# Performance work log

Hardware: AMD Instinct MI355X
Metric: run time of the kernel (lower is better)

The kernel has to match this reference:

```python
import jax, jax.numpy as jnp
import numpy as np

K_CLUSTERS = 64   # hardcoded k=64 in get_kmenas_prototypes
KM_ITERS = 10     # KMeans(max_iter=10)


def _kmeans_one_hot(x):
    """x: (B, N, C) points. Returns one-hot cluster masks (B, K, N)."""
    B, N, C = x.shape
    init_idx = jnp.round(jnp.linspace(0, N - 1, K_CLUSTERS)).astype(jnp.int32)

    def per_item(pts):  # (N, C)
        p2 = (pts * pts).sum(-1)  # (N,)

        def assign(cent):
            c2 = (cent * cent).sum(-1)
            d = p2[:, None] + c2[None, :] - 2.0 * (pts @ cent.T)  # (N, K)
            return jnp.argmin(d, axis=1)

        def step(i, cent):
            lab = assign(cent)
            oh = jax.nn.one_hot(lab, K_CLUSTERS, dtype=pts.dtype)  # (N, K)
            cnt = oh.sum(0)
            sums = oh.T @ pts  # (K, C)
            return jnp.where(cnt[:, None] > 0, sums / jnp.maximum(cnt, 1.0)[:, None], cent)

        cent = jax.lax.fori_loop(0, KM_ITERS, step, pts[init_idx])
        lab = assign(cent)
        return jax.nn.one_hot(lab, K_CLUSTERS, dtype=pts.dtype).T  # (K, N)

    return jax.vmap(per_item)(x)


def reference(target, ref, sqz_w, sqz_b, slot_w, slot_b, Wq, Wk, Wv, Wo):
    B, Cin, H, W = target.shape
    Cout = sqz_w.shape[0]
    R = ref.shape[0]
    HW = H * W

    # 1x1 convs
    sqz_target = jnp.einsum('bchw,oc->bohw', target, sqz_w) + sqz_b[None, :, None, None]
    slot_target = jnp.einsum('bchw,oc->bohw', target, slot_w) + slot_b[None, :, None, None]

    xt = sqz_target.reshape(B, Cout, HW)  # (B, C, HW)

    # KMeans prototypes (clustering mask is detached in the original)
    mask = jax.lax.stop_gradient(_kmeans_one_hot(xt.transpose(0, 2, 1)))  # (B, K, HW)
    target_pt = jnp.einsum('bkn,bcn->bkc', mask, xt)  # (B, K, C)

    # slot prototypes: softmax over slot/channel dim (dim=1)
    ss = jax.nn.softmax(slot_target.reshape(B, -1, HW), axis=1)  # (B, S, HW)
    slot_pt = jnp.einsum('bsn,bcn->bsc', ss, xt)  # (B, S, C)
    slot_mask = ss.reshape(B, -1, H, W)

    # ref prototypes: mask = feature itself, softmax over spatial dim (dim=2)
    sqz_ref = jnp.einsum('rbchw,oc->rbohw', ref, sqz_w) + sqz_b[None, None, :, None, None]
    xr = sqz_ref.reshape(R, B, Cout, HW)
    ssr = jax.nn.softmax(xr, axis=3)
    ref_pt = jnp.einsum('rbcn,rbdn->rbcd', ssr, xr)  # (R, B, C, C)

    # Feature_Aggregation_Transformer: cross-attention, queries = kmeans tokens,
    # kv = flattened ref prototype tokens (b, R*C, C)
    kv = ref_pt.transpose(1, 0, 2, 3).reshape(B, R * Cout, Cout)
    q = target_pt @ Wq
    k = kv @ Wk
    v = kv @ Wv
    scale = 1.0 / jnp.sqrt(jnp.asarray(Cout, q.dtype))
    attn = jax.nn.softmax(jnp.einsum('bqc,bkc->bqk', q, k) * scale, axis=-1)
    agg_pt = jnp.einsum('bqk,bkc->bqc', attn, v) @ Wo + target_pt  # (B, K, C)

    return (sqz_target, agg_pt, ref_pt, slot_pt, slot_mask)


def setup_inputs() -> dict:
    key = jax.random.key(0)
    ks = jax.random.split(key, 12)
    B, Cin, Cout, S, H, W, R = 8, 512, 128, 16, 64, 64, 3
    w = lambda k, shp: (jax.random.normal(k, shp, dtype=jnp.float32) * 0.02)
    return {
        'target': jax.random.normal(ks[0], (B, Cin, H, W), dtype=jnp.float32),
        'ref': jax.random.normal(ks[1], (R, B, Cin, H, W), dtype=jnp.float32),
        'sqz_w': w(ks[2], (Cout, Cin)),
        'sqz_b': jnp.zeros((Cout,), dtype=jnp.float32),
        'slot_w': w(ks[3], (S, Cin)),
        'slot_b': jnp.zeros((S,), dtype=jnp.float32),
        'Wq': w(ks[4], (Cout, Cout)),
        'Wk': w(ks[5], (Cout, Cout)),
        'Wv': w(ks[6], (Cout, Cout)),
        'Wo': w(ks[7], (Cout, Cout)),
    }
```

## Files before the change

### kernel.cpp

```cpp
#include <hip/hip_runtime.h>

#define NB 8
#define CIN 512
#define CO 128
#define NS 16
#define NHW 4096
#define NR 3
#define NK 64
#define KMITERS 10

typedef __attribute__((ext_vector_type(8))) short s16x8;
typedef __attribute__((ext_vector_type(4))) float f32x4;

static __device__ __forceinline__ void bsplit(float x, short& h, short& l) {
    union { float f; unsigned u; } a; a.f = x;
    h = (short)(a.u >> 16);
    union { unsigned u; float f; } hf; hf.u = a.u & 0xFFFF0000u;
    union { float f; unsigned u; } r; r.f = x - hf.f;
    l = (short)(r.u >> 16);
}

__global__ __launch_bounds__(256) void conv_mfma(const float* __restrict__ X,
    const float* __restrict__ Wt, const float* __restrict__ bias, float* __restrict__ out)
{
    __shared__ short sWh[128 * 40];
    __shared__ short sWl[128 * 40];
    __shared__ float sX[32 * 133];
    const int g = blockIdx.y;
    const int n0 = blockIdx.x * 128;
    const int tid = threadIdx.x;
    const int lane = tid & 63, w = tid >> 6;
    const int l15 = lane & 15, quad = lane >> 4;
    const int wm = (w & 1) * 64, wn = (w >> 1) * 64;

    f32x4 acc[4][4];
#pragma unroll
    for (int i = 0; i < 4; ++i)
#pragma unroll
        for (int j = 0; j < 4; ++j) acc[i][j] = (f32x4){0.f, 0.f, 0.f, 0.f};

    for (int c0 = 0; c0 < CIN; c0 += 32) {
        if (c0) __syncthreads();
#pragma unroll
        for (int r = 0; r < 4; ++r) {
            int e = r * 1024 + tid * 4;
            int m = e >> 5, cc = e & 31;
            const float4 wv = *(const float4*)&Wt[(size_t)m * CIN + c0 + cc];
            short h0, l0, h1, l1, h2, l2, h3, l3;
            bsplit(wv.x, h0, l0); bsplit(wv.y, h1, l1);
            bsplit(wv.z, h2, l2); bsplit(wv.w, h3, l3);
            *(short4*)&sWh[m * 40 + cc] = make_short4(h0, h1, h2, h3);
            *(short4*)&sWl[m * 40 + cc] = make_short4(l0, l1, l2, l3);
        }
#pragma unroll
        for (int r = 0; r < 4; ++r) {
            int e = r * 1024 + tid * 4;
            int k = e >> 7, n = e & 127;
            const float4 xv = *(const float4*)&X[((size_t)g * CIN + c0 + k) * NHW + n0 + n];
            float* p = &sX[k * 133 + n];
            p[0] = xv.x; p[1] = xv.y; p[2] = xv.z; p[3] = xv.w;
        }
        __syncthreads();

        s16x8 ah[4], al[4];
#pragma unroll
        for (int mt = 0; mt < 4; ++mt) {
            int m = wm + mt * 16 + l15;
            ah[mt] = *(const s16x8*)&sWh[m * 40 + quad * 8];
            al[mt] = *(const s16x8*)&sWl[m * 40 + quad * 8];
        }
#pragma unroll
        for (int nt = 0; nt < 4; ++nt) {
            int n = wn + nt * 16 + l15;
            s16x8 bh, bl;
#pragma unroll
            for (int jj = 0; jj < 8; ++jj) {
                float xv = sX[(quad * 8 + jj) * 133 + n];
                short h, l; bsplit(xv, h, l);
                bh[jj] = h; bl[jj] = l;
            }
#pragma unroll
            for (int mt = 0; mt < 4; ++mt) {
                acc[mt][nt] = __builtin_amdgcn_mfma_f32_16x16x32_bf16(ah[mt], bh, acc[mt][nt], 0, 0, 0);
                acc[mt][nt] = __builtin_amdgcn_mfma_f32_16x16x32_bf16(ah[mt], bl, acc[mt][nt], 0, 0, 0);
                acc[mt][nt] = __builtin_amdgcn_mfma_f32_16x16x32_bf16(al[mt], bh, acc[mt][nt], 0, 0, 0);
            }
        }
    }
#pragma unroll
    for (int mt = 0; mt < 4; ++mt) {
#pragma unroll
        for (int reg = 0; reg < 4; ++reg) {
            int m = wm + mt * 16 + quad * 4 + reg;
            float bv = bias[m];
#pragma unroll
            for (int nt = 0; nt < 4; ++nt) {
                int n = wn + nt * 16 + l15;
                out[((size_t)g * CO + m) * NHW + n0 + n] = acc[mt][nt][reg] + bv;
            }
        }
    }
}

template<int BM, int BN, int BK, int TM, int TN>
__global__ __launch_bounds__(256) void conv1x1(const float* __restrict__ X,
    const float* __restrict__ Wt, const float* __restrict__ bias,
    float* __restrict__ outf)
{
    static_assert(TM == 4 && (TN == 4 || TN == 8), "mapping assumes TM=4");
    __shared__ float sW[BK][BM + 4];
    __shared__ float sX2[BK][BN + 4];
    const int g  = blockIdx.z;
    const int m0 = blockIdx.y * BM;
    const int n0 = blockIdx.x * BN;
    const int tid = threadIdx.x;
    constexpr int NTH_N = BN / TN;
    const int tn = tid % NTH_N;
    const int tm = tid / NTH_N;
    const int O = gridDim.y * BM;
    const int cb0 = tn * 4;
    const int cb1 = BN / 2 + tn * 4;

    float acc[TM][TN];
#pragma unroll
    for (int i = 0; i < TM; ++i)
#pragma unroll
        for (int j = 0; j < TN; ++j) acc[i][j] = 0.f;

    for (int c0 = 0; c0 < CIN; c0 += BK) {
        if (c0) __syncthreads();
        constexpr int F4R = BK / 4;
        for (int idx4 = tid; idx4 < BM * F4R; idx4 += 256) {
            int m = idx4 / F4R, cw = (idx4 % F4R) * 4;
            const float4 wv = *(const float4*)&Wt[(size_t)(m0 + m) * CIN + c0 + cw];
            sW[cw][m] = wv.x; sW[cw + 1][m] = wv.y;
            sW[cw + 2][m] = wv.z; sW[cw + 3][m] = wv.w;
        }
        constexpr int F4N = BN / 4;
        for (int idx4 = tid; idx4 < BK * F4N; idx4 += 256) {
            int k = idx4 / F4N, n4 = (idx4 % F4N) * 4;
            *(float4*)&sX2[k][n4] =
                *(const float4*)&X[((size_t)g * CIN + c0 + k) * NHW + n0 + n4];
        }
        __syncthreads();
#pragma unroll
        for (int k = 0; k < BK; ++k) {
            float a[TM], bb[TN];
            *(float4*)&a[0] = *(const float4*)&sW[k][tm * 4];
            *(float4*)&bb[0] = *(const float4*)&sX2[k][cb0];
            if constexpr (TN == 8)
                *(float4*)&bb[4] = *(const float4*)&sX2[k][cb1];
#pragma unroll
            for (int i = 0; i < TM; ++i)
#pragma unroll
                for (int j = 0; j < TN; ++j) acc[i][j] = fmaf(a[i], bb[j], acc[i][j]);
        }
    }
#pragma unroll
    for (int i = 0; i < TM; ++i) {
        int m = m0 + tm * 4 + i;
        float bv = bias[m];
        float4 o0;
        o0.x = acc[i][0] + bv; o0.y = acc[i][1] + bv;
        o0.z = acc[i][2] + bv; o0.w = acc[i][3] + bv;
        *(float4*)&outf[((size_t)g * O + m) * NHW + n0 + cb0] = o0;
        if constexpr (TN == 8) {
            float4 o1;
            o1.x = acc[i][4] + bv; o1.y = acc[i][5] + bv;
            o1.z = acc[i][6] + bv; o1.w = acc[i][7] + bv;
            *(float4*)&outf[((size_t)g * O + m) * NHW + n0 + cb1] = o1;
        }
    }
}

__global__ void km_init(const float* __restrict__ xt, float* __restrict__ cent) {
    int idx = blockIdx.x * 256 + threadIdx.x;
    if (idx >= NB * NK * CO) return;
    int c = idx % CO;
    int k = (idx / CO) % NK;
    int b = idx / (CO * NK);
    cent[idx] = xt[((size_t)b * CO + c) * NHW + 65 * k];
}

__global__ __launch_bounds__(1024) void km_label(const float* __restrict__ xt,
    const float* __restrict__ cent, float* __restrict__ psums, float* __restrict__ pcnt)
{
    __shared__ float sCent[64 * 129];
    __shared__ float sXs[128 * 133];
    __shared__ float sC2[64];
    __shared__ float sCnt[64];
    __shared__ int sLab[128];
    const int b = blockIdx.y, nb = blockIdx.x;
    const int n0 = nb * 128;
    const int tid = threadIdx.x;

#pragma unroll
    for (int r = 0; r < 2; ++r) {
        int e = r * 4096 + tid * 4;
        int k = e >> 7, c = e & 127;
        const float4 cv = *(const float4*)&cent[((size_t)b * NK + k) * CO + c];
        float* p = &sCent[k * 129 + c];
        p[0] = cv.x; p[1] = cv.y; p[2] = cv.z; p[3] = cv.w;
    }
#pragma unroll
    for (int r = 0; r < 4; ++r) {
        int e = r * 4096 + tid * 4;
        int c = e >> 7, n = e & 127;
        const float4 xv = *(const float4*)&xt[((size_t)b * CO + c) * NHW + n0 + n];
        float* p = &sXs[c * 133 + n];
        p[0] = xv.x; p[1] = xv.y; p[2] = xv.z; p[3] = xv.w;
    }
    __syncthreads();
    if (tid < 64) {
        float s = 0.f;
        for (int c = 0; c < CO; ++c) { float v = sCent[tid * 129 + c]; s = fmaf(v, v, s); }
        sC2[tid] = s;
    }
    __syncthreads();

    const int tn = tid & 7, tm = tid >> 3;
    float dot[8];
    float p2 = 0.f;
#pragma unroll
    for (int j = 0; j < 8; ++j) dot[j] = 0.f;
    for (int cc = 0; cc < 4; ++cc) {
        for (int c4 = 0; c4 < 8; ++c4) {
            float xv[4];
#pragma unroll
            for (int j = 0; j < 4; ++j)
                xv[j] = sXs[(cc * 32 + c4 * 4 + j) * 133 + tm];
#pragma unroll
            for (int j = 0; j < 4; ++j)
                p2 = fmaf(xv[j], xv[j], p2);
#pragma unroll
            for (int jj = 0; jj < 8; ++jj) {
                int k = tn * 8 + jj;
#pragma unroll
                for (int j = 0; j < 4; ++j) {
                    float cv = sCent[k * 129 + cc * 32 + c4 * 4 + j];
                    dot[jj] = fmaf(xv[j], cv, dot[jj]);
                }
            }
        }
    }
    {
        int lab = tn * 8;
        float bd = p2 + sC2[tn * 8] - 2.f * dot[0];
#pragma unroll
        for (int jj = 1; jj < 8; ++jj) {
            int k = tn * 8 + jj;
            float d = p2 + sC2[k] - 2.f * dot[jj];
            if (d < bd) { bd = d; lab = k; }
        }
#pragma unroll
        for (int off = 1; off < 8; off <<= 1) {
            float d2 = __shfl_xor(bd, off);
            int l2 = __shfl_xor(lab, off);
            if (d2 < bd || (d2 == bd && l2 < lab)) { bd = d2; lab = l2; }
        }
        if (tn == 0) sLab[tm] = lab;
    }
    __syncthreads();
    for (int e = tid; e < 64 * 129; e += 1024) sCent[e] = 0.f;
    if (tid < 64) sCnt[tid] = 0.f;
    __syncthreads();
    if (tid < 128) atomicAdd(&sCnt[sLab[tid]], 1.f);
    if (tid < 256) {
        const int cq = tid & 31, sh = tid >> 5;
        for (int cc = 0; cc < 4; ++cc) {
            int c = cc * 32 + cq;
            for (int ii = 0; ii < 16; ++ii) {
                int p = sh * 16 + ii;
                atomicAdd(&sCent[sLab[p] * 129 + c], sXs[c * 133 + p]);
            }
        }
    }
    __syncthreads();
    float* ps = &psums[((size_t)b * 32 + nb) * (NK * CO)];
    for (int e = tid; e < NK * CO; e += 1024) {
        int k = e >> 7, c = e & 127;
        ps[e] = sCent[k * 129 + c];
    }
    if (tid < 64) pcnt[((size_t)b * 32 + nb) * 64 + tid] = sCnt[tid];
}

__global__ void km_update2(float* __restrict__ cent, float* __restrict__ tpt,
    const float* __restrict__ psums, const float* __restrict__ pcnt, int mode)
{
    const int k = blockIdx.x, b = blockIdx.y, c = threadIdx.x;
    float s = 0.f;
    for (int nb = 0; nb < 32; ++nb)
        s += psums[((size_t)b * 32 + nb) * (NK * CO) + k * CO + c];
    if (mode) { tpt[((size_t)b * NK + k) * CO + c] = s; return; }
    float cn = 0.f;
    for (int nb = 0; nb < 32; ++nb)
        cn += pcnt[((size_t)b * 32 + nb) * 64 + k];
    if (cn > 0.f) cent[((size_t)b * NK + k) * CO + c] = s / fmaxf(cn, 1.f);
}

__global__ void slot_softmax(const float* __restrict__ ssb, float* __restrict__ out4) {
    int idx = blockIdx.x * 256 + threadIdx.x;
    if (idx >= NB * NHW) return;
    int b = idx / NHW, n = idx % NHW;
    float v[NS];
    float m = -1e30f;
#pragma unroll
    for (int s = 0; s < NS; ++s) { v[s] = ssb[((size_t)b * NS + s) * NHW + n]; m = fmaxf(m, v[s]); }
    float sum = 0.f;
#pragma unroll
    for (int s = 0; s < NS; ++s) { v[s] = expf(v[s] - m); sum += v[s]; }
    float inv = 1.f / sum;
#pragma unroll
    for (int s = 0; s < NS; ++s)
        out4[((size_t)b * NS + s) * NHW + n] = v[s] * inv;
}

__global__ __launch_bounds__(256) void slot_pt_kernel(const float* __restrict__ ss,
    const float* __restrict__ xt, float* __restrict__ spt)
{
    __shared__ float sS[NS][257];
    __shared__ float sX2[32][257];
    const int b = blockIdx.y;
    const int n0 = blockIdx.x * 256;
    const int tid = threadIdx.x;
    for (int i = tid; i < NS * 256; i += 256) {
        int s = i >> 8, nn = i & 255;
        sS[s][nn] = ss[((size_t)b * NS + s) * NHW + n0 + nn];
    }
    const int c = tid & 31;
    const int sA = tid >> 5;
    for (int cg = 0; cg < 4; ++cg) {
        __syncthreads();
        for (int i = tid; i < 32 * 256; i += 256) {
            int cc = i >> 8, nn = i & 255;
            sX2[cc][nn] = xt[((size_t)b * CO + cg * 32 + cc) * NHW + n0 + nn];
        }
        __syncthreads();
        float a0 = 0.f, a1 = 0.f;
        for (int nn = 0; nn < 256; ++nn) {
            float x = sX2[c][nn];
            a0 = fmaf(x, sS[sA][nn], a0);
            a1 = fmaf(x, sS[sA + 8][nn], a1);
        }
        atomicAdd(&spt[((size_t)b * NS + sA) * CO + cg * 32 + c], a0);
        atomicAdd(&spt[((size_t)b * NS + sA + 8) * CO + cg * 32 + c], a1);
    }
}

__global__ __launch_bounds__(256) void rowstats(const float* __restrict__ xr,
    float* __restrict__ rmax, float* __restrict__ rinv)
{
    const int row = blockIdx.x;
    const float* p = xr + (size_t)row * NHW;
    const int tid = threadIdx.x;
    float v[16];
    float m = -1e30f;
#pragma unroll
    for (int i = 0; i < 16; ++i) { v[i] = p[tid + (i << 8)]; m = fmaxf(m, v[i]); }
#pragma unroll
    for (int off = 32; off; off >>= 1) m = fmaxf(m, __shfl_down(m, off));
    __shared__ float sm[4];
    __shared__ float ss2[4];
    const int wid = tid >> 6, lane = tid & 63;
    if (lane == 0) sm[wid] = m;
    __syncthreads();
    m = fmaxf(fmaxf(sm[0], sm[1]), fmaxf(sm[2], sm[3]));
    float s = 0.f;
#pragma unroll
    for (int i = 0; i < 16; ++i) s += expf(v[i] - m);
#pragma unroll
    for (int off = 32; off; off >>= 1) s += __shfl_down(s, off);
    if (lane == 0) ss2[wid] = s;
    __syncthreads();
    if (tid == 0) {
        rmax[row] = m;
        rinv[row] = 1.f / (ss2[0] + ss2[1] + ss2[2] + ss2[3]);
    }
}

__global__ __launch_bounds__(256) void refpt_mfma(const float* __restrict__ xr,
    const float* __restrict__ rmax, const float* __restrict__ rinv,
    float* __restrict__ refpt)
{
    __shared__ short sSh[128 * 40];
    __shared__ short sSl[128 * 40];
    __shared__ short sXh[128 * 40];
    __shared__ short sXl[128 * 40];
    __shared__ float sMax[CO];
    __shared__ float sInv[CO];
    const int g = blockIdx.y;
    const int n0 = blockIdx.x * 256;
    const int tid = threadIdx.x;
    const int lane = tid & 63, w = tid >> 6;
    const int l15 = lane & 15, quad = lane >> 4;
    const int wm = (w & 1) * 64, wn = (w >> 1) * 64;
    const float* base = xr + (size_t)g * CO * NHW;

    if (tid < CO) {
        sMax[tid] = rmax[g * CO + tid];
        sInv[tid] = rinv[g * CO + tid];
    }

    f32x4 acc[4][4];
#pragma unroll
    for (int i = 0; i < 4; ++i)
#pragma unroll
        for (int j = 0; j < 4; ++j) acc[i][j] = (f32x4){0.f, 0.f, 0.f, 0.f};

    for (int ks = 0; ks < 8; ++ks) {
        __syncthreads();
#pragma unroll
        for (int r = 0; r < 4; ++r) {
            int e = r * 1024 + tid * 4;
            int row = e >> 5, col = e & 31;
            const float4 xv = *(const float4*)&base[(size_t)row * NHW + n0 + ks * 32 + col];
            const float mx = sMax[row], iv = sInv[row];
            short h0, l0, h1, l1, h2, l2, h3, l3;
            bsplit(xv.x, h0, l0); bsplit(xv.y, h1, l1);
            bsplit(xv.z, h2, l2); bsplit(xv.w, h3, l3);
            *(short4*)&sXh[row * 40 + col] = make_short4(h0, h1, h2, h3);
            *(short4*)&sXl[row * 40 + col] = make_short4(l0, l1, l2, l3);
            float s0 = expf(xv.x - mx) * iv, s1 = expf(xv.y - mx) * iv;
            float s2 = expf(xv.z - mx) * iv, s3 = expf(xv.w - mx) * iv;
            bsplit(s0, h0, l0); bsplit(s1, h1, l1);
            bsplit(s2, h2, l2); bsplit(s3, h3, l3);
            *(short4*)&sSh[row * 40 + col] = make_short4(h0, h1, h2, h3);
            *(short4*)&sSl[row * 40 + col] = make_short4(l0, l1, l2, l3);
        }
        __syncthreads();

        s16x8 ah[4], al[4];
#pragma unroll
        for (int mt = 0; mt < 4; ++mt) {
            int m = wm + mt * 16 + l15;
            ah[mt] = *(const s16x8*)&sSh[m * 40 + quad * 8];
            al[mt] = *(const s16x8*)&sSl[m * 40 + quad * 8];
        }
#pragma unroll
        for (int nt = 0; nt < 4; ++nt) {
            int d = wn + nt * 16 + l15;
            s16x8 bh = *(const s16x8*)&sXh[d * 40 + quad * 8];
            s16x8 bl = *(const s16x8*)&sXl[d * 40 + quad * 8];
#pragma unroll
            for (int mt = 0; mt < 4; ++mt) {
                acc[mt][nt] = __builtin_amdgcn_mfma_f32_16x16x32_bf16(ah[mt], bh, acc[mt][nt], 0, 0, 0);
                acc[mt][nt] = __builtin_amdgcn_mfma_f32_16x16x32_bf16(ah[mt], bl, acc[mt][nt], 0, 0, 0);
                acc[mt][nt] = __builtin_amdgcn_mfma_f32_16x16x32_bf16(al[mt], bh, acc[mt][nt], 0, 0, 0);
            }
        }
    }
#pragma unroll
    for (int mt = 0; mt < 4; ++mt) {
#pragma unroll
        for (int reg = 0; reg < 4; ++reg) {
            int m = wm + mt * 16 + quad * 4 + reg;
#pragma unroll
            for (int nt = 0; nt < 4; ++nt) {
                int d = wn + nt * 16 + l15;
                atomicAdd(&refpt[((size_t)g * CO + m) * CO + d], acc[mt][nt][reg]);
            }
        }
    }
}

__global__ void build_kv(const float* __restrict__ refpt, float* __restrict__ kv) {
    int idx = blockIdx.x * 256 + threadIdx.x;
    if (idx >= NB * NR * CO * CO) return;
    int d = idx % CO;
    int j = (idx / CO) % (NR * CO);
    int b = idx / (CO * NR * CO);
    int r = j / CO, cc = j % CO;
    kv[idx] = refpt[(((size_t)r * NB + b) * CO + cc) * CO + d];
}

__global__ void gemm_aw(const float* __restrict__ A, const float* __restrict__ Wm,
                        float* __restrict__ Cm, int M)
{
    int idx = blockIdx.x * 256 + threadIdx.x;
    if (idx >= NB * M * CO) return;
    int c = idx % CO;
    int m = (idx / CO) % M;
    int b = idx / (CO * M);
    const float* ar = A + ((size_t)b * M + m) * CO;
    float acc = 0.f;
    for (int e = 0; e < CO; ++e) acc = fmaf(ar[e], Wm[e * CO + c], acc);
    Cm[idx] = acc;
}

__global__ __launch_bounds__(256) void attn_kernel(const float* __restrict__ qb,
    const float* __restrict__ kb, const float* __restrict__ vb, float* __restrict__ ctx)
{
    __shared__ float sq[CO];
    __shared__ float sl[NR * CO];
    __shared__ float red[4], red2[4];
    const int b = blockIdx.y, i = blockIdx.x;
    const int tid = threadIdx.x;
    if (tid < CO) sq[tid] = qb[((size_t)b * NK + i) * CO + tid];
    __syncthreads();
    const float scale = 0.08838834764831843f;
    for (int j = tid; j < NR * CO; j += 256) {
        const float* kr = kb + ((size_t)b * NR * CO + j) * CO;
        float d = 0.f;
        for (int e = 0; e < CO; ++e) d = fmaf(sq[e], kr[e], d);
        sl[j] = d * scale;
    }
    __syncthreads();
    float m = -1e30f;
    for (int j = tid; j < NR * CO; j += 256) m = fmaxf(m, sl[j]);
#pragma unroll
    for (int off = 32; off; off >>= 1) m = fmaxf(m, __shfl_down(m, off));
    if ((tid & 63) == 0) red[tid >> 6] = m;
    __syncthreads();
    m = fmaxf(fmaxf(red[0], red[1]), fmaxf(red[2], red[3]));
    float s = 0.f;
    for (int j = tid; j < NR * CO; j += 256) { float e = expf(sl[j] - m); sl[j] = e; s += e; }
#pragma unroll
    for (int off = 32; off; off >>= 1) s += __shfl_down(s, off);
    if ((tid & 63) == 0) red2[tid >> 6] = s;
    __syncthreads();
    const float inv = 1.f / (red2[0] + red2[1] + red2[2] + red2[3]);
    if (tid < CO) {
        float acc = 0.f;
        for (int j = 0; j < NR * CO; ++j)
            acc = fmaf(sl[j], vb[((size_t)b * NR * CO + j) * CO + tid], acc);
        ctx[((size_t)b * NK + i) * CO + tid] = acc * inv;
    }
}

__global__ void final_agg(const float* __restrict__ ctx, const float* __restrict__ Wo,
                          const float* __restrict__ tpt, float* __restrict__ out1)
{
    int idx = blockIdx.x * 256 + threadIdx.x;
    if (idx >= NB * NK * CO) return;
    int c = idx % CO;
    const float* cr = ctx + (size_t)(idx / CO) * CO;
    float acc = tpt[idx];
    for (int e = 0; e < CO; ++e) acc = fmaf(cr[e], Wo[e * CO + c], acc);
    out1[idx] = acc;
}

extern "C" void kernel_launch(void* const* d_in, const int* in_sizes, int n_in,
                              void* d_out, int out_size, void* d_ws, size_t ws_size,
                              hipStream_t stream) {
    (void)in_sizes; (void)n_in; (void)out_size; (void)ws_size;
    const float* target = (const float*)d_in[0];
    const float* ref    = (const float*)d_in[1];
    const float* sqz_w  = (const float*)d_in[2];
    const float* sqz_b  = (const float*)d_in[3];
    const float* slot_w = (const float*)d_in[4];
    const float* slot_b = (const float*)d_in[5];
    const float* Wq     = (const float*)d_in[6];
    const float* Wk     = (const float*)d_in[7];
    const float* Wv     = (const float*)d_in[8];
    const float* Wo     = (const float*)d_in[9];

    float* out  = (float*)d_out;
    float* out0 = out;
    float* out1 = out + 4194304;
    float* out2 = out + 4259840;
    float* out3 = out + 4653056;
    float* out4 = out + 4669440;

    float* ws    = (float*)d_ws;
    float* ssb   = ws;
    float* xr    = ssb + 524288;
    float* rmax  = xr + 12582912;
    float* rinv  = rmax + 3072;
    float* cent  = rinv + 3072;
    float* psums = cent + 65536;
    float* pcnt  = psums + 2097152;
    float* tpt   = pcnt + 16384;
    float* kvb   = tpt + 65536;
    float* qb    = kvb + 393216;
    float* kb    = qb + 65536;
    float* vb    = kb + 393216;
    float* ctxb  = vb + 393216;

    hipMemsetAsync(out3, 0, (size_t)16384 * 4, stream);
    hipMemsetAsync(out2, 0, (size_t)393216 * 4, stream);

    conv1x1<64, 128, 32, 4, 8><<<dim3(NHW / 128, CO / 64, NB), 256, 0, stream>>>(
        target, sqz_w, sqz_b, out0);
    conv1x1<16, 256, 32, 4, 4><<<dim3(NHW / 256, 1, NB), 256, 0, stream>>>(
        target, slot_w, slot_b, ssb);
    conv_mfma<<<dim3(NHW / 128, NR * NB), 256, 0, stream>>>(ref, sqz_w, sqz_b, xr);

    km_init<<<(NB * NK * CO + 255) / 256, 256, 0, stream>>>(out0, cent);
    for (int it = 0; it < KMITERS; ++it) {
        km_label<<<dim3(32, NB), 1024, 0, stream>>>(out0, cent, psums, pcnt);
        km_update2<<<dim3(NK, NB), 128, 0, stream>>>(cent, tpt, psums, pcnt, 0);
    }
    km_label<<<dim3(32, NB), 1024, 0, stream>>>(out0, cent, psums, pcnt);
    km_update2<<<dim3(NK, NB), 128, 0, stream>>>(cent, tpt, psums, pcnt, 1);

    slot_softmax<<<(NB * NHW + 255) / 256, 256, 0, stream>>>(ssb, out4);
    slot_pt_kernel<<<dim3(NHW / 256, NB), 256, 0, stream>>>(out4, out0, out3);

    rowstats<<<NR * NB * CO, 256, 0, stream>>>(xr, rmax, rinv);
    refpt_mfma<<<dim3(NHW / 256, NR * NB), 256, 0, stream>>>(xr, rmax, rinv, out2);

    build_kv<<<(NB * NR * CO * CO + 255) / 256, 256, 0, stream>>>(out2, kvb);
    gemm_aw<<<(NB * NK * CO + 255) / 256, 256, 0, stream>>>(tpt, Wq, qb, NK);
    gemm_aw<<<(NB * NR * CO * CO + 255) / 256, 256, 0, stream>>>(kvb, Wk, kb, NR * CO);
    gemm_aw<<<(NB * NR * CO * CO + 255) / 256, 256, 0, stream>>>(kvb, Wv, vb, NR * CO);
    attn_kernel<<<dim3(NK, NB), 256, 0, stream>>>(qb, kb, vb, ctxb);
    final_agg<<<(NB * NK * CO + 255) / 256, 256, 0, stream>>>(ctxb, Wo, tpt, out1);
}
```

Before: 1.323 ms.

## Pre-split conv weights to bf16 pairs and register-tile kmeans label kernel

A small kernel now splits the squeeze weights into bf16 high and low halves once, so conv_mfma loads those halves directly instead of re-splitting every weight tile in every block. The activation tile is also split at staging time and stored as packed hi/lo words, so the inner MFMA loop no longer repeats the split per n-tile. km_label moves to 512 threads with a 4x4 register tile of points by centroids, vectorized LDS reads, a padded centroid layout, and a 32-channel slice of points staged at a time. That shrinks shared memory but reloads the point tile twice from global, once for distances and once for accumulating sums.

```diff
diff --git a/kernel.cpp b/kernel.cpp
--- a/kernel.cpp
+++ b/kernel.cpp
@@ -20,12 +20,23 @@
     l = (short)(r.u >> 16);
 }
 
+__global__ void split_w(const float* __restrict__ Wt,
+    unsigned short* __restrict__ Whi, unsigned short* __restrict__ Wlo)
+{
+    int idx = blockIdx.x * 256 + threadIdx.x;
+    if (idx >= CO * CIN) return;
+    short h, l; bsplit(Wt[idx], h, l);
+    Whi[idx] = (unsigned short)h;
+    Wlo[idx] = (unsigned short)l;
+}
+
 __global__ __launch_bounds__(256) void conv_mfma(const float* __restrict__ X,
-    const float* __restrict__ Wt, const float* __restrict__ bias, float* __restrict__ out)
+    const unsigned short* __restrict__ Whi, const unsigned short* __restrict__ Wlo,
+    const float* __restrict__ bias, float* __restrict__ out)
 {
     __shared__ short sWh[128 * 40];
     __shared__ short sWl[128 * 40];
-    __shared__ float sX[32 * 133];
+    __shared__ unsigned sXp[32 * 133];
     const int g = blockIdx.y;
     const int n0 = blockIdx.x * 128;
     const int tid = threadIdx.x;
@@ -42,23 +53,25 @@
     for (int c0 = 0; c0 < CIN; c0 += 32) {
         if (c0) __syncthreads();
 #pragma unroll
-        for (int r = 0; r < 4; ++r) {
-            int e = r * 1024 + tid * 4;
+        for (int r = 0; r < 2; ++r) {
+            int e = (r * 256 + tid) * 8;
             int m = e >> 5, cc = e & 31;
-            const float4 wv = *(const float4*)&Wt[(size_t)m * CIN + c0 + cc];
-            short h0, l0, h1, l1, h2, l2, h3, l3;
-            bsplit(wv.x, h0, l0); bsplit(wv.y, h1, l1);
-            bsplit(wv.z, h2, l2); bsplit(wv.w, h3, l3);
-            *(short4*)&sWh[m * 40 + cc] = make_short4(h0, h1, h2, h3);
-            *(short4*)&sWl[m * 40 + cc] = make_short4(l0, l1, l2, l3);
+            *(int4*)&sWh[m * 40 + cc] = *(const int4*)&Whi[(size_t)m * CIN + c0 + cc];
+            *(int4*)&sWl[m * 40 + cc] = *(const int4*)&Wlo[(size_t)m * CIN + c0 + cc];
         }
 #pragma unroll
         for (int r = 0; r < 4; ++r) {
             int e = r * 1024 + tid * 4;
             int k = e >> 7, n = e & 127;
             const float4 xv = *(const float4*)&X[((size_t)g * CIN + c0 + k) * NHW + n0 + n];
-            float* p = &sX[k * 133 + n];
-            p[0] = xv.x; p[1] = xv.y; p[2] = xv.z; p[3] = xv.w;
+            short h0, l0, h1, l1, h2, l2, h3, l3;
+            bsplit(xv.x, h0, l0); bsplit(xv.y, h1, l1);
+            bsplit(xv.z, h2, l2); bsplit(xv.w, h3, l3);
+            unsigned* p = &sXp[k * 133 + n];
+            p[0] = ((unsigned)(unsigned short)h0 << 16) | (unsigned short)l0;
+            p[1] = ((unsigned)(unsigned short)h1 << 16) | (unsigned short)l1;
+            p[2] = ((unsigned)(unsigned short)h2 << 16) | (unsigned short)l2;
+            p[3] = ((unsigned)(unsigned short)h3 << 16) | (unsigned short)l3;
         }
         __syncthreads();
 
@@ -75,9 +88,9 @@
             s16x8 bh, bl;
 #pragma unroll
             for (int jj = 0; jj < 8; ++jj) {
-                float xv = sX[(quad * 8 + jj) * 133 + n];
-                short h, l; bsplit(xv, h, l);
-                bh[jj] = h; bl[jj] = l;
+                unsigned v = sXp[(quad * 8 + jj) * 133 + n];
+                bh[jj] = (short)(v >> 16);
+                bl[jj] = (short)(v & 0xffffu);
             }
 #pragma unroll
             for (int mt = 0; mt < 4; ++mt) {
@@ -182,11 +195,13 @@
     cent[idx] = xt[((size_t)b * CO + c) * NHW + 65 * k];
 }
 
-__global__ __launch_bounds__(1024) void km_label(const float* __restrict__ xt,
+#define CIDX(k, c) ((k) * 136 + (((k) >> 3) << 2) + (c))
+
+__global__ __launch_bounds__(512) void km_label(const float* __restrict__ xt,
     const float* __restrict__ cent, float* __restrict__ psums, float* __restrict__ pcnt)
 {
-    __shared__ float sCent[64 * 129];
-    __shared__ float sXs[128 * 133];
+    __shared__ float sCent[8736];
+    __shared__ float sXs[32 * 132];
     __shared__ float sC2[64];
     __shared__ float sCnt[64];
     __shared__ int sLab[128];
@@ -195,91 +210,106 @@
     const int tid = threadIdx.x;
 
 #pragma unroll
-    for (int r = 0; r < 2; ++r) {
-        int e = r * 4096 + tid * 4;
+    for (int r = 0; r < 4; ++r) {
+        int e = r * 2048 + tid * 4;
         int k = e >> 7, c = e & 127;
-        const float4 cv = *(const float4*)&cent[((size_t)b * NK + k) * CO + c];
-        float* p = &sCent[k * 129 + c];
-        p[0] = cv.x; p[1] = cv.y; p[2] = cv.z; p[3] = cv.w;
-    }
-#pragma unroll
-    for (int r = 0; r < 4; ++r) {
-        int e = r * 4096 + tid * 4;
-        int c = e >> 7, n = e & 127;
-        const float4 xv = *(const float4*)&xt[((size_t)b * CO + c) * NHW + n0 + n];
-        float* p = &sXs[c * 133 + n];
-        p[0] = xv.x; p[1] = xv.y; p[2] = xv.z; p[3] = xv.w;
+        *(f32x4*)&sCent[CIDX(k, c)] = *(const f32x4*)&cent[((size_t)b * NK + k) * CO + c];
     }
     __syncthreads();
     if (tid < 64) {
         float s = 0.f;
-        for (int c = 0; c < CO; ++c) { float v = sCent[tid * 129 + c]; s = fmaf(v, v, s); }
+        for (int c = 0; c < CO; ++c) { float v = sCent[CIDX(tid, c)]; s = fmaf(v, v, s); }
         sC2[tid] = s;
     }
-    __syncthreads();
-
-    const int tn = tid & 7, tm = tid >> 3;
-    float dot[8];
-    float p2 = 0.f;
-#pragma unroll
-    for (int j = 0; j < 8; ++j) dot[j] = 0.f;
+
+    const int tn = tid & 15, tm = tid >> 4;
+    float dot[4][4];
+    float p2[4];
+#pragma unroll
+    for (int i = 0; i < 4; ++i) {
+        p2[i] = 0.f;
+#pragma unroll
+        for (int j = 0; j < 4; ++j) dot[i][j] = 0.f;
+    }
     for (int cc = 0; cc < 4; ++cc) {
+        __syncthreads();
+#pragma unroll
+        for (int r = 0; r < 2; ++r) {
+            int e = r * 2048 + tid * 4;
+            int c = e >> 7, n = e & 127;
+            *(f32x4*)&sXs[c * 132 + n] =
+                *(const f32x4*)&xt[((size_t)b * CO + cc * 32 + c) * NHW + n0 + n];
+        }
+        __syncthreads();
         for (int c4 = 0; c4 < 8; ++c4) {
-            float xv[4];
+            f32x4 xf[4];
 #pragma unroll
             for (int j = 0; j < 4; ++j)
-                xv[j] = sXs[(cc * 32 + c4 * 4 + j) * 133 + tm];
+                xf[j] = *(const f32x4*)&sXs[(c4 * 4 + j) * 132 + tm * 4];
 #pragma unroll
             for (int j = 0; j < 4; ++j)
-                p2 = fmaf(xv[j], xv[j], p2);
-#pragma unroll
-            for (int jj = 0; jj < 8; ++jj) {
-                int k = tn * 8 + jj;
-#pragma unroll
-                for (int j = 0; j < 4; ++j) {
-                    float cv = sCent[k * 129 + cc * 32 + c4 * 4 + j];
-                    dot[jj] = fmaf(xv[j], cv, dot[jj]);
-                }
+#pragma unroll
+                for (int i = 0; i < 4; ++i)
+                    p2[i] = fmaf(xf[j][i], xf[j][i], p2[i]);
+#pragma unroll
+            for (int jj = 0; jj < 4; ++jj) {
+                int k = tn * 4 + jj;
+                f32x4 cf = *(const f32x4*)&sCent[CIDX(k, cc * 32 + c4 * 4)];
+#pragma unroll
+                for (int j = 0; j < 4; ++j)
+#pragma unroll
+                    for (int i = 0; i < 4; ++i)
+                        dot[i][jj] = fmaf(xf[j][i], cf[j], dot[i][jj]);
             }
         }
     }
-    {
-        int lab = tn * 8;
-        float bd = p2 + sC2[tn * 8] - 2.f * dot[0];
-#pragma unroll
-        for (int jj = 1; jj < 8; ++jj) {
-            int k = tn * 8 + jj;
-            float d = p2 + sC2[k] - 2.f * dot[jj];
+#pragma unroll
+    for (int i = 0; i < 4; ++i) {
+        int lab = tn * 4;
+        float bd = p2[i] + sC2[tn * 4] - 2.f * dot[i][0];
+#pragma unroll
+        for (int jj = 1; jj < 4; ++jj) {
+            int k = tn * 4 + jj;
+            float d = p2[i] + sC2[k] - 2.f * dot[i][jj];
             if (d < bd) { bd = d; lab = k; }
         }
 #pragma unroll
-        for (int off = 1; off < 8; off <<= 1) {
+        for (int off = 1; off < 16; off <<= 1) {
             float d2 = __shfl_xor(bd, off);
             int l2 = __shfl_xor(lab, off);
             if (d2 < bd || (d2 == bd && l2 < lab)) { bd = d2; lab = l2; }
         }
-        if (tn == 0) sLab[tm] = lab;
-    }
-    __syncthreads();
-    for (int e = tid; e < 64 * 129; e += 1024) sCent[e] = 0.f;
+        if (tn == 0) sLab[tm * 4 + i] = lab;
+    }
+    __syncthreads();
+    for (int e = tid; e < 8736; e += 512) sCent[e] = 0.f;
     if (tid < 64) sCnt[tid] = 0.f;
     __syncthreads();
     if (tid < 128) atomicAdd(&sCnt[sLab[tid]], 1.f);
-    if (tid < 256) {
-        const int cq = tid & 31, sh = tid >> 5;
-        for (int cc = 0; cc < 4; ++cc) {
+    for (int cc = 0; cc < 4; ++cc) {
+        __syncthreads();
+#pragma unroll
+        for (int r = 0; r < 2; ++r) {
+            int e = r * 2048 + tid * 4;
+            int c = e >> 7, n = e & 127;
+            *(f32x4*)&sXs[c * 132 + n] =
+                *(const f32x4*)&xt[((size_t)b * CO + cc * 32 + c) * NHW + n0 + n];
+        }
+        __syncthreads();
+        if (tid < 256) {
+            const int cq = tid & 31, sh = tid >> 5;
             int c = cc * 32 + cq;
             for (int ii = 0; ii < 16; ++ii) {
                 int p = sh * 16 + ii;
-                atomicAdd(&sCent[sLab[p] * 129 + c], sXs[c * 133 + p]);
+                atomicAdd(&sCent[CIDX(sLab[p], c)], sXs[cq * 132 + p]);
             }
         }
     }
     __syncthreads();
     float* ps = &psums[((size_t)b * 32 + nb) * (NK * CO)];
-    for (int e = tid; e < NK * CO; e += 1024) {
+    for (int e = tid; e < NK * CO; e += 512) {
         int k = e >> 7, c = e & 127;
-        ps[e] = sCent[k * 129 + c];
+        ps[e] = sCent[CIDX(k, c)];
     }
     if (tid < 64) pcnt[((size_t)b * 32 + nb) * 64 + tid] = sCnt[tid];
 }
@@ -575,22 +605,25 @@
     float* kb    = qb + 65536;
     float* vb    = kb + 393216;
     float* ctxb  = vb + 393216;
+    unsigned short* Whi = (unsigned short*)(ctxb + 65536);
+    unsigned short* Wlo = Whi + CO * CIN;
 
     hipMemsetAsync(out3, 0, (size_t)16384 * 4, stream);
     hipMemsetAsync(out2, 0, (size_t)393216 * 4, stream);
 
+    split_w<<<(CO * CIN + 255) / 256, 256, 0, stream>>>(sqz_w, Whi, Wlo);
     conv1x1<64, 128, 32, 4, 8><<<dim3(NHW / 128, CO / 64, NB), 256, 0, stream>>>(
         target, sqz_w, sqz_b, out0);
     conv1x1<16, 256, 32, 4, 4><<<dim3(NHW / 256, 1, NB), 256, 0, stream>>>(
         target, slot_w, slot_b, ssb);
-    conv_mfma<<<dim3(NHW / 128, NR * NB), 256, 0, stream>>>(ref, sqz_w, sqz_b, xr);
+    conv_mfma<<<dim3(NHW / 128, NR * NB), 256, 0, stream>>>(ref, Whi, Wlo, sqz_b, xr);
 
     km_init<<<(NB * NK * CO + 255) / 256, 256, 0, stream>>>(out0, cent);
     for (int it = 0; it < KMITERS; ++it) {
-        km_label<<<dim3(32, NB), 1024, 0, stream>>>(out0, cent, psums, pcnt);
+        km_label<<<dim3(32, NB), 512, 0, stream>>>(out0, cent, psums, pcnt);
         km_update2<<<dim3(NK, NB), 128, 0, stream>>>(cent, tpt, psums, pcnt, 0);
     }
-    km_label<<<dim3(32, NB), 1024, 0, stream>>>(out0, cent, psums, pcnt);
+    km_label<<<dim3(32, NB), 512, 0, stream>>>(out0, cent, psums, pcnt);
     km_update2<<<dim3(NK, NB), 128, 0, stream>>>(cent, tpt, psums, pcnt, 1);
 
     slot_softmax<<<(NB * NHW + 255) / 256, 256, 0, stream>>>(ssb, out4);
```

New measurement: 1.126 ms. -14.9%, faster.
